# Optimization experiments

Measured on AMD Instinct MI355X. Metric: run time of the kernel, lower is better.

Reference implementation:

```python
import jax, jax.numpy as jnp
import numpy as np

TOPK = 16
MIN_SIM = 0.05
MIN_VOTES = 0.3
REMOVE_INNER = 0.5
NUM_CLASSES = 1000


def setup_inputs() -> dict:
    key = jax.random.key(0)
    kq, kdb, kid, kxy, kwh = jax.random.split(key, 5)
    Qn, N, C = 1024, 200000, 256
    q = jax.random.normal(kq, (Qn, C), dtype=jnp.float32)
    q = q / jnp.linalg.norm(q, axis=1, keepdims=True)
    db = jax.random.normal(kdb, (N, C), dtype=jnp.float32)
    db = db / jnp.linalg.norm(db, axis=1, keepdims=True)
    ids = jax.random.randint(kid, (N,), 0, NUM_CLASSES).astype(jnp.float32)
    places_db = jnp.concatenate([db, ids[:, None]], axis=1)  # (N, C+1)
    xy = jax.random.uniform(kxy, (Qn, 2), minval=0.0, maxval=800.0)
    wh = jax.random.uniform(kwh, (Qn, 2), minval=10.0, maxval=200.0)
    boxes = jnp.concatenate([xy, xy + wh], axis=1)  # valid xyxy boxes
    return {"boxes": boxes, "descriptors": q, "places_db": places_db}


def _remove_overlapping_boxes(boxes, labels, thr):
    # overlap = intersection / min(area_i, area_j); drop the BIGGER box of any
    # same-label pair whose overlap >= thr.
    bf = boxes.astype(jnp.float32)
    x1, y1, x2, y2 = bf[:, 0], bf[:, 1], bf[:, 2], bf[:, 3]
    areas = (x2 - x1) * (y2 - y1)
    xi1 = jnp.maximum(x1[:, None], x1[None, :])
    yi1 = jnp.maximum(y1[:, None], y1[None, :])
    xi2 = jnp.minimum(x2[:, None], x2[None, :])
    yi2 = jnp.minimum(y2[:, None], y2[None, :])
    inter = jnp.clip(xi2 - xi1, 0.0) * jnp.clip(yi2 - yi1, 0.0)
    area_i, area_j = areas[:, None], areas[None, :]
    area_small = jnp.minimum(area_i, area_j)
    overlap = jnp.where(area_small > 0, inter / jnp.maximum(area_small, 1e-12), 0.0)
    same_lbl = (labels[:, None] == labels[None, :]) & (labels[:, None] >= 0)
    n = boxes.shape[0]
    non_diag = ~jnp.eye(n, dtype=bool)
    mask_pair = same_lbl & (overlap >= thr) & non_diag
    bigger_i = area_i > area_j
    remove_i = (mask_pair & bigger_i).any(axis=1)
    remove_j = (mask_pair & ~bigger_i).any(axis=0)
    remove = remove_i | remove_j
    return jnp.where(remove, jnp.full_like(labels, -1), labels)


def reference(boxes, descriptors, places_db):
    X = places_db[:, :-1]                       # (N, C)
    ids = places_db[:, -1].astype(jnp.int32)    # (N,)
    sims = descriptors @ X.T                    # (Q, N)
    top_sims, top_idx = jax.lax.top_k(sims, TOPK)   # (Q, topk)
    top_ids = ids[top_idx]                          # (Q, topk)
    mask_sim = top_sims >= MIN_SIM
    # one-hot majority vote over classes
    one_hot = (top_ids[:, :, None] == jnp.arange(NUM_CLASSES, dtype=jnp.int32)[None, None, :]).astype(jnp.float32)
    vote_counts = (one_hot * mask_sim[:, :, None].astype(jnp.float32)).sum(axis=1)  # (Q, NUM_CLASSES)
    majority_counts = vote_counts.max(axis=1)
    majority_ids = jnp.argmax(vote_counts, axis=1).astype(jnp.int32)
    valid_votes = mask_sim.sum(axis=1).astype(jnp.float32)
    vote_ratio = jnp.where(valid_votes > 0, majority_counts / jnp.maximum(valid_votes, 1.0), 0.0)
    valid = (majority_counts > 0) & (vote_ratio >= MIN_VOTES)
    results = jnp.where(valid, majority_ids, jnp.full_like(majority_ids, -1))
    results = _remove_overlapping_boxes(boxes, results, REMOVE_INNER)
    match = (top_ids == results[:, None]) & mask_sim
    sim_scores = jnp.where(match, top_sims, jnp.zeros_like(top_sims)).max(axis=1)
    valid_mask = (results >= 0) & jnp.isfinite(sim_scores) & jnp.isfinite(boxes).all(axis=1)
    # Static-shape variant of the original's compaction: invalid rows are
    # marked with class=-1 / score=0 instead of being sliced out.
    return (boxes,
            jnp.where(valid_mask, sim_scores, 0.0),
            jnp.where(valid_mask, results, -1))
```

## Files before the change

kernel.cpp:

```cpp
#include <hip/hip_runtime.h>
#include <hip/hip_bf16.h>

#define QN 1024
#define NDB 200000
#define NDB_PAD 200064
#define PDBW 257
#define CDIM 256
#define TK 16
#define NEGF (-1e30f)
#define MIN_SIM_C 0.05f
#define MIN_VOTES_C 0.3f

#define NCH 128
#define THETA 0.19f
#define CAPQ 14
#define NCHUNK1 49
#define CPQ1 (NCHUNK1*32)

typedef __attribute__((ext_vector_type(8))) short bf16x8;
typedef __attribute__((ext_vector_type(4))) float f32x4;
typedef __attribute__((ext_vector_type(8))) int   i32x8;
typedef __attribute__((ext_vector_type(4))) int   i32x4;

__device__ __forceinline__ short f2bf(float f) {
  union { float f; unsigned u; } x; x.f = f;
  unsigned u = x.u;
  return (short)((u + 0x7fffu + ((u >> 16) & 1u)) >> 16);
}

__device__ __forceinline__ unsigned pk_fp8x4(float a, float b, float c, float d) {
  unsigned w = (unsigned)__builtin_amdgcn_cvt_pk_fp8_f32(a, b, 0, false);
  w = (unsigned)__builtin_amdgcn_cvt_pk_fp8_f32(c, d, (int)w, true);
  return w;
}

__global__ __launch_bounds__(512, 1) void sims_fused_kernel(
    const float* __restrict__ qd, const float* __restrict__ pdb,
    unsigned long long* __restrict__ seg_g, unsigned int* __restrict__ cnt_g,
    int* __restrict__ flag)
{
  __shared__ __align__(16) char db_lds[2][64 * 256];
  __shared__ unsigned seg_lds[8][64][CAPQ][2];
  __shared__ int lcnt[8][64];

  const int tid  = (int)threadIdx.x;
  const int lane = tid & 63;
  const int wv   = tid >> 6;
  const int cid  = (int)blockIdx.x;
  const int mt   = (int)blockIdx.y;
  const int nsub = 24 + (cid < 54 ? 1 : 0);
  const int row0 = (24*cid + (cid < 54 ? cid : 54)) << 6;

  if (cid == 0 && mt == 0 && tid == 0) *flag = 0;
  lcnt[wv][lane] = 0;

  const int l15  = lane & 15;
  const int egrp = lane >> 4;
  const int rowb = egrp << 2;
  const int colb = l15;

  const int srow = tid >> 3;
  const int sp   = tid & 7;
  const int sg0  = ((2*sp    ) ^ (srow & 15)) << 4;
  const int sg1  = ((2*sp + 1) ^ (srow & 15)) << 4;
  const int sbase = srow * 256;

  i32x8 aq[4][2];
  {
    #pragma unroll
    for (int fm = 0; fm < 4; ++fm) {
      const float* qrow = qd + (size_t)(mt*512 + wv*64 + fm*16 + l15)*CDIM;
      #pragma unroll
      for (int kk = 0; kk < 2; ++kk) {
        const float* p = qrow + kk*128 + egrp*32;
        i32x8 a;
        #pragma unroll
        for (int d = 0; d < 8; ++d) {
          float4 x = *(const float4*)(p + d*4);
          a[d] = (int)pk_fp8x4(x.x, x.y, x.z, x.w);
        }
        aq[fm][kk] = a;
      }
    }
  }

  float4 sf0, sf1, sf2, sf3, sf4, sf5, sf6, sf7;
#define LOADT(tile) do { \
    const int _r = row0 + (tile)*64 + srow; \
    if (_r < NDB) { \
      const float* _p = pdb + (size_t)_r*PDBW + sp*32; \
      sf0 = *(const float4*)(_p);      sf1 = *(const float4*)(_p + 4); \
      sf2 = *(const float4*)(_p + 8);  sf3 = *(const float4*)(_p + 12); \
      sf4 = *(const float4*)(_p + 16); sf5 = *(const float4*)(_p + 20); \
      sf6 = *(const float4*)(_p + 24); sf7 = *(const float4*)(_p + 28); \
    } else { \
      sf0 = sf1 = sf2 = sf3 = sf4 = sf5 = sf6 = sf7 = (float4){0.f, 0.f, 0.f, 0.f}; \
    } \
  } while (0)
#define STAGEW(bufi) do { \
    i32x4 _w0, _w1; \
    _w0[0] = (int)pk_fp8x4(sf0.x, sf0.y, sf0.z, sf0.w); \
    _w0[1] = (int)pk_fp8x4(sf1.x, sf1.y, sf1.z, sf1.w); \
    _w0[2] = (int)pk_fp8x4(sf2.x, sf2.y, sf2.z, sf2.w); \
    _w0[3] = (int)pk_fp8x4(sf3.x, sf3.y, sf3.z, sf3.w); \
    _w1[0] = (int)pk_fp8x4(sf4.x, sf4.y, sf4.z, sf4.w); \
    _w1[1] = (int)pk_fp8x4(sf5.x, sf5.y, sf5.z, sf5.w); \
    _w1[2] = (int)pk_fp8x4(sf6.x, sf6.y, sf6.z, sf6.w); \
    _w1[3] = (int)pk_fp8x4(sf7.x, sf7.y, sf7.z, sf7.w); \
    *(i32x4*)(db_lds[(bufi)] + sbase + sg0) = _w0; \
    *(i32x4*)(db_lds[(bufi)] + sbase + sg1) = _w1; \
  } while (0)

  LOADT(0);
  STAGEW(0);
  LOADT(1);
  __syncthreads();

  for (int s = 0; s < nsub; ++s) {
    if (s + 1 < nsub) {
      STAGEW((s + 1) & 1);
      if (s + 2 < nsub) LOADT(s + 2);
    }

    f32x4 acc[4][4];
    #pragma unroll
    for (int fm = 0; fm < 4; ++fm)
      #pragma unroll
      for (int fn = 0; fn < 4; ++fn)
        acc[fm][fn] = (f32x4){0.f, 0.f, 0.f, 0.f};
    __builtin_amdgcn_s_setprio(1);
    {
      const char* dbt = (const char*)db_lds[s & 1];
      #pragma unroll
      for (int kk = 0; kk < 2; ++kk) {
        #pragma unroll
        for (int fn = 0; fn < 4; ++fn) {
          const char* rowp = dbt + (fn*16 + l15)*256;
          const int mbase = kk*8 + egrp*2;
          i32x4 lo = *(const i32x4*)(rowp + (((mbase    ) ^ l15) << 4));
          i32x4 hi = *(const i32x4*)(rowp + (((mbase + 1) ^ l15) << 4));
          i32x8 b = __builtin_shufflevector(lo, hi, 0, 1, 2, 3, 4, 5, 6, 7);
          #pragma unroll
          for (int fm = 0; fm < 4; ++fm)
            acc[fm][fn] = __builtin_amdgcn_mfma_scale_f32_16x16x128_f8f6f4(
                aq[fm][kk], b, acc[fm][fn],
                0 , 0 ,
                0, 0x7F7F7F7Fu , 0, 0x7F7F7F7Fu );
        }
      }
    }
    __builtin_amdgcn_s_setprio(0);

    {
      const int idxbase = row0 + s*64;
      #pragma unroll
      for (int fm = 0; fm < 4; ++fm)
        #pragma unroll
        for (int fn = 0; fn < 4; ++fn) {
          const f32x4 a = acc[fm][fn];
          const float m = fmaxf(fmaxf(a[0], a[1]), fmaxf(a[2], a[3]));
          if (m > THETA) {
            #pragma unroll
            for (int j = 0; j < 4; ++j) {
              if (a[j] > THETA) {
                const int ql = fm*16 + rowb + j;
                const int slot = atomicAdd(&lcnt[wv][ql], 1);
                if (slot < CAPQ) {
                  seg_lds[wv][ql][slot][0] = __float_as_uint(a[j]);
                  seg_lds[wv][ql][slot][1] = (unsigned)(idxbase + fn*16 + colb);
                }
              }
            }
          }
        }
    }

    asm volatile("s_waitcnt lgkmcnt(0)" ::: "memory");
    __builtin_amdgcn_sched_barrier(0);
    __builtin_amdgcn_s_barrier();
    __builtin_amdgcn_sched_barrier(0);
  }
#undef LOADT
#undef STAGEW

  {
    const int cnt = lcnt[wv][lane];
    const int qg = mt*512 + wv*64 + lane;
    cnt_g[qg*NCH + cid] = (unsigned)cnt;
    const int nc = min(cnt, CAPQ);
    unsigned long long* dst = seg_g + (size_t)(qg*NCH + cid)*CAPQ;
    for (int j = 0; j < nc; ++j) {
      unsigned long long lo = seg_lds[wv][lane][j][0];
      unsigned long long hi = seg_lds[wv][lane][j][1];
      dst[j] = lo | (hi << 32);
    }
  }
}

__global__ __launch_bounds__(64) void gather_vote_kernel(
    const float* __restrict__ pdb,
    const unsigned long long* __restrict__ seg_g, const unsigned* __restrict__ cnt_g,
    int* __restrict__ out_label, float* __restrict__ out_s, int* __restrict__ flag)
{
  __shared__ float    cv[NCH*CAPQ];
  __shared__ unsigned ci[NCH*CAPQ];
  const int q    = (int)blockIdx.x;
  const int lane = (int)threadIdx.x;

  bool over = false;
  int tot = 0;
  #pragma unroll
  for (int h = 0; h < NCH/64; ++h) {
    const int c = h*64 + lane;
    const int cnt = (int)cnt_g[q*NCH + c];
    over |= (cnt > CAPQ);
    const int nc = min(cnt, CAPQ);
    tot += nc;
    const unsigned long long* src = seg_g + (size_t)(q*NCH + c)*CAPQ;
    for (int j = 0; j < CAPQ; ++j) {
      float v = NEGF; unsigned idx = 0u;
      if (j < nc) {
        const unsigned long long e = src[j];
        v = __uint_as_float((unsigned)e);
        idx = (unsigned)(e >> 32);
      }
      cv[c*CAPQ + j] = v;
      ci[c*CAPQ + j] = idx;
    }
  }
  #pragma unroll
  for (int off = 32; off >= 1; off >>= 1) tot += __shfl_xor(tot, off);
  __syncthreads();

  float topv[TK]; int topid[TK];
  #pragma unroll
  for (int r = 0; r < TK; ++r) {
    float bv = NEGF; int bp = -1;
    #pragma unroll 4
    for (int j = 0; j < (NCH*CAPQ)/64; ++j) {
      const int p = j*64 + lane;
      const float v = cv[p];
      if (v > bv) { bv = v; bp = p; }
    }
    #pragma unroll
    for (int off = 32; off >= 1; off >>= 1) {
      const float ov = __shfl_xor(bv, off);
      const int   op = __shfl_xor(bp, off);
      if (ov > bv || (ov == bv && ((unsigned)op < (unsigned)bp))) { bv = ov; bp = op; }
    }
    topv[r] = bv;
    int id = -2;
    if (bp >= 0 && bv > NEGF) id = (int)pdb[(size_t)ci[bp]*PDBW + CDIM];
    topid[r] = id;
    if (lane == 0 && bp >= 0) cv[bp] = NEGF;
    __syncthreads();
  }

  if (lane == 0) {
    bool mk[TK];
    int nvalid = 0;
    #pragma unroll
    for (int i = 0; i < TK; ++i) {
      mk[i] = (topv[i] >= MIN_SIM_C) && (topid[i] >= 0);
      nvalid += mk[i] ? 1 : 0;
    }
    int maj = 0, majid = 0x7fffffff;
    for (int i = 0; i < TK; ++i) {
      if (!mk[i]) continue;
      int c = 0;
      for (int j = 0; j < TK; ++j) c += (mk[j] && topid[j] == topid[i]) ? 1 : 0;
      if (c > maj || (c == maj && topid[i] < majid)) { maj = c; majid = topid[i]; }
    }
    const float ratio = (float)maj / fmaxf((float)nvalid, 1.0f);
    const bool valid = (maj > 0) && (ratio >= MIN_VOTES_C);
    const int label = valid ? majid : -1;
    float s = 0.f;
    #pragma unroll
    for (int i = 0; i < TK; ++i)
      if (mk[i] && topid[i] == label) s = fmaxf(s, topv[i]);
    out_label[q] = label;
    out_s[q]     = s;
  }
  const bool bad = (__ballot(over) != 0ull) || (tot < TK);
  if (lane == 0 && bad) atomicOr(flag, 1);
}

__global__ __launch_bounds__(256, 2) void sims_topk1_kernel(
    const float* __restrict__ qd, const float* __restrict__ pdb,
    float* __restrict__ cand_val, unsigned int* __restrict__ cand_idx,
    const int* __restrict__ gate)
{
  if (gate && *gate == 0) return;
  __shared__ __align__(16) short db_lds[128 * 264];
  float* sims = (float*)db_lds;

  const int tid  = (int)threadIdx.x;
  const int lane = tid & 63;
  const int wv   = tid >> 6;
  const int cid   = (int)blockIdx.x;
  const int mtile = (int)blockIdx.y;

  bf16x8 aq[2][8];
  {
    const int l15 = lane & 15;
    const int kb  = (lane >> 4) << 3;
    #pragma unroll
    for (int fm = 0; fm < 2; ++fm) {
      const int row = mtile*128 + wv*32 + fm*16 + l15;
      #pragma unroll
      for (int kk = 0; kk < 8; ++kk) {
        const float* p = qd + (size_t)row*CDIM + kk*32 + kb;
        float4 x0 = *(const float4*)p;
        float4 x1 = *(const float4*)(p + 4);
        bf16x8 a;
        a[0]=f2bf(x0.x); a[1]=f2bf(x0.y); a[2]=f2bf(x0.z); a[3]=f2bf(x0.w);
        a[4]=f2bf(x1.x); a[5]=f2bf(x1.y); a[6]=f2bf(x1.z); a[7]=f2bf(x1.w);
        aq[fm][kk] = a;
      }
    }
  }

  float    tv[TK];
  unsigned ti[TK];
  #pragma unroll
  for (int i = 0; i < TK; ++i) { tv[i] = NEGF; ti[i] = 0u; }
  float minv = NEGF; int minp = 0;

  const int g0chunk = cid * 4096;
  const int q_l  = tid & 127;
  const int half = tid >> 7;

  for (int s = 0; s < 32; ++s) {
    const int g0 = g0chunk + s*128;
    {
      const int rb = tid >> 6;
      const int c4 = (tid & 63) << 2;
      for (int i = 0; i < 32; ++i) {
        const int rl = i*4 + rb;
        const int g  = g0 + rl;
        float v0, v1, v2, v3;
        if (g < NDB) {
          const float* p = pdb + (size_t)g*PDBW + c4;
          v0 = p[0]; v1 = p[1]; v2 = p[2]; v3 = p[3];
        } else { v0 = v1 = v2 = v3 = 0.f; }
        short* d = &db_lds[rl*264 + c4];
        d[0]=f2bf(v0); d[1]=f2bf(v1); d[2]=f2bf(v2); d[3]=f2bf(v3);
      }
    }
    __syncthreads();

    f32x4 acc[2][8];
    #pragma unroll
    for (int fm = 0; fm < 2; ++fm)
      #pragma unroll
      for (int fn = 0; fn < 8; ++fn)
        acc[fm][fn] = (f32x4){0.f, 0.f, 0.f, 0.f};
    {
      const int l15 = lane & 15;
      const int kb  = (lane >> 4) << 3;
      #pragma unroll
      for (int kk = 0; kk < 8; ++kk) {
        bf16x8 b[8];
        #pragma unroll
        for (int fn = 0; fn < 8; ++fn)
          b[fn] = *(const bf16x8*)&db_lds[(fn*16 + l15)*264 + kk*32 + kb];
        #pragma unroll
        for (int fn = 0; fn < 8; ++fn) {
          acc[0][fn] = __builtin_amdgcn_mfma_f32_16x16x32_bf16(aq[0][kk], b[fn], acc[0][fn], 0, 0, 0);
          acc[1][fn] = __builtin_amdgcn_mfma_f32_16x16x32_bf16(aq[1][kk], b[fn], acc[1][fn], 0, 0, 0);
        }
      }
    }
    __syncthreads();

    {
      const int colb = lane & 15;
      const int rowb = (lane >> 4) << 2;
      #pragma unroll
      for (int fm = 0; fm < 2; ++fm)
        #pragma unroll
        for (int fn = 0; fn < 8; ++fn)
          #pragma unroll
          for (int j = 0; j < 4; ++j)
            sims[(wv*32 + fm*16 + rowb + j)*129 + fn*16 + colb] = acc[fm][fn][j];
    }
    __syncthreads();

    {
      const int cb = half * 64;
      #pragma unroll 4
      for (int c = 0; c < 64; ++c) {
        const int colc = cb + c;
        const float v = sims[q_l*129 + colc];
        const int g = g0 + colc;
        if (v > minv && g < NDB) {
          #pragma unroll
          for (int i = 0; i < TK; ++i) if (i == minp) { tv[i] = v; ti[i] = (unsigned)g; }
          minv = tv[0]; minp = 0;
          #pragma unroll
          for (int i = 1; i < TK; ++i) if (tv[i] < minv) { minv = tv[i]; minp = i; }
        }
      }
    }
    __syncthreads();
  }

  {
    const int qg = mtile*128 + q_l;
    float*    pv = cand_val + ((size_t)qg*NCHUNK1 + cid)*32 + half*TK;
    unsigned* pi = cand_idx + ((size_t)qg*NCHUNK1 + cid)*32 + half*TK;
    #pragma unroll
    for (int i = 0; i < TK; ++i) { pv[i] = tv[i]; pi[i] = ti[i]; }
  }
}

template<int CPQ>
__global__ __launch_bounds__(64) void merge_vote_kernel(
    const float* __restrict__ pdb,
    const float* __restrict__ cand_val, const unsigned* __restrict__ cand_idx,
    int* __restrict__ out_label, float* __restrict__ out_s,
    const int* __restrict__ gate)
{
  if (gate && *gate == 0) return;
  __shared__ float    cv[CPQ];
  __shared__ unsigned ci[CPQ];
  const int q    = (int)blockIdx.x;
  const int lane = (int)threadIdx.x;

  for (int j = lane; j < CPQ; j += 64) {
    cv[j] = cand_val[(size_t)q*CPQ + j];
    ci[j] = cand_idx[(size_t)q*CPQ + j];
  }
  __syncthreads();

  float topv[TK]; int topid[TK];
  #pragma unroll
  for (int r = 0; r < TK; ++r) {
    float bv = NEGF; int bp = -1;
    for (int j = lane; j < CPQ; j += 64) {
      const float v = cv[j];
      if (v > bv) { bv = v; bp = j; }
    }
    #pragma unroll
    for (int off = 32; off >= 1; off >>= 1) {
      const float ov = __shfl_xor(bv, off);
      const int   op = __shfl_xor(bp, off);
      if (ov > bv || (ov == bv && ((unsigned)op < (unsigned)bp))) { bv = ov; bp = op; }
    }
    topv[r] = bv;
    int id = -2;
    if (bp >= 0 && bv > NEGF) id = (int)pdb[(size_t)ci[bp]*PDBW + CDIM];
    topid[r] = id;
    if (lane == 0 && bp >= 0) cv[bp] = NEGF;
    __syncthreads();
  }

  if (lane == 0) {
    bool mk[TK];
    int nvalid = 0;
    #pragma unroll
    for (int i = 0; i < TK; ++i) {
      mk[i] = (topv[i] >= MIN_SIM_C) && (topid[i] >= 0);
      nvalid += mk[i] ? 1 : 0;
    }
    int maj = 0, majid = 0x7fffffff;
    for (int i = 0; i < TK; ++i) {
      if (!mk[i]) continue;
      int c = 0;
      for (int j = 0; j < TK; ++j) c += (mk[j] && topid[j] == topid[i]) ? 1 : 0;
      if (c > maj || (c == maj && topid[i] < majid)) { maj = c; majid = topid[i]; }
    }
    const float ratio = (float)maj / fmaxf((float)nvalid, 1.0f);
    const bool valid = (maj > 0) && (ratio >= MIN_VOTES_C);
    const int label = valid ? majid : -1;
    float s = 0.f;
    #pragma unroll
    for (int i = 0; i < TK; ++i)
      if (mk[i] && topid[i] == label) s = fmaxf(s, topv[i]);
    out_label[q] = label;
    out_s[q]     = s;
  }
}

__device__ __forceinline__ bool finitef(float v) {
  return ((__float_as_uint(v) >> 23) & 0xffu) != 0xffu;
}

__global__ __launch_bounds__(64) void finalize_kernel(
    const float* __restrict__ boxes, const int* __restrict__ labels,
    const float* __restrict__ svals, float* __restrict__ out)
{
  const int x    = (int)blockIdx.x;
  const int lane = (int)threadIdx.x;
  const int lx = labels[x];
  const float bx1 = boxes[x*4+0], by1 = boxes[x*4+1];
  const float bx2 = boxes[x*4+2], by2 = boxes[x*4+3];
  const float ax = (bx2 - bx1) * (by2 - by1);

  bool flag = false;
  if (lx >= 0) {
    for (int y = lane; y < QN; y += 64) {
      if (y == x) continue;
      if (labels[y] != lx) continue;
      const float c1 = boxes[y*4+0], c2 = boxes[y*4+1];
      const float c3 = boxes[y*4+2], c4 = boxes[y*4+3];
      const float ay = (c3 - c1) * (c4 - c2);
      const float xi1 = fmaxf(bx1, c1), yi1 = fmaxf(by1, c2);
      const float xi2 = fminf(bx2, c3), yi2 = fminf(by2, c4);
      const float inter = fmaxf(xi2 - xi1, 0.f) * fmaxf(yi2 - yi1, 0.f);
      const float asmall = fminf(ax, ay);
      const float ov = (asmall > 0.f) ? inter / fmaxf(asmall, 1e-12f) : 0.f;
      if (ov >= 0.5f && ay <= ax) flag = true;
    }
  }
  const bool removed = (__ballot(flag) != 0ull);
  const int label = removed ? -1 : lx;
  const float s = svals[x];
  const bool fin = finitef(s) && finitef(bx1) && finitef(by1) && finitef(bx2) && finitef(by2);
  const bool valid = (label >= 0) && fin;

  if (lane == 0) {
    out[4096 + x] = valid ? s : 0.f;
    out[5120 + x] = (float)(valid ? label : -1);
  }
  if (lane < 4) out[x*4 + lane] = boxes[x*4 + lane];
}

extern "C" void kernel_launch(void* const* d_in, const int* in_sizes, int n_in,
                              void* d_out, int out_size, void* d_ws, size_t ws_size,
                              hipStream_t stream)
{
  const float* boxes = (const float*)d_in[0];
  const float* qd    = (const float*)d_in[1];
  const float* pdb   = (const float*)d_in[2];
  float* out = (float*)d_out;
  char* ws = (char*)d_ws;

  const size_t seg_bytes = (size_t)QN * NCH * CAPQ * 8;
  const size_t cnt_bytes = (size_t)QN * NCH * 4;
  const size_t c1_bytes  = (size_t)QN * CPQ1 * 8;
  const size_t A_bytes   = (seg_bytes + cnt_bytes > c1_bytes) ? seg_bytes + cnt_bytes : c1_bytes;
  const size_t need = A_bytes + (size_t)QN*8 + 64;

  if (ws_size >= need) {
    char* A = ws;
    unsigned long long* seg_g = (unsigned long long*)A;
    unsigned*           cnt_g = (unsigned*)(A + seg_bytes);
    float*    cand_val = (float*)A;
    unsigned* cand_idx = (unsigned*)(A + (size_t)QN*CPQ1*4);
    int*      labels   = (int*)(ws + A_bytes);
    float*    svals    = (float*)(ws + A_bytes + (size_t)QN*4);
    int*      flag     = (int*)(ws + A_bytes + (size_t)QN*8);

    hipLaunchKernelGGL(sims_fused_kernel, dim3(NCH, 2), dim3(512), 0, stream,
                       qd, pdb, seg_g, cnt_g, flag);
    hipLaunchKernelGGL(gather_vote_kernel, dim3(QN), dim3(64), 0, stream,
                       pdb, seg_g, cnt_g, labels, svals, flag);
    hipLaunchKernelGGL(sims_topk1_kernel, dim3(NCHUNK1, 8), dim3(256), 0, stream,
                       qd, pdb, cand_val, cand_idx, flag);
    hipLaunchKernelGGL((merge_vote_kernel<CPQ1>), dim3(QN), dim3(64), 0, stream,
                       pdb, cand_val, cand_idx, labels, svals, flag);
    hipLaunchKernelGGL(finalize_kernel, dim3(QN), dim3(64), 0, stream,
                       boxes, labels, svals, out);
  } else {
    const size_t n1 = (size_t)QN * CPQ1;
    float*    cand_val = (float*)ws;
    unsigned* cand_idx = (unsigned*)(ws + n1*4);
    int*      labels   = (int*)(ws + n1*8);
    float*    svals    = (float*)(ws + n1*8 + (size_t)QN*4);

    hipLaunchKernelGGL(sims_topk1_kernel, dim3(NCHUNK1, 8), dim3(256), 0, stream,
                       qd, pdb, cand_val, cand_idx, (const int*)nullptr);
    hipLaunchKernelGGL((merge_vote_kernel<CPQ1>), dim3(QN), dim3(64), 0, stream,
                       pdb, cand_val, cand_idx, labels, svals, (const int*)nullptr);
    hipLaunchKernelGGL(finalize_kernel, dim3(QN), dim3(64), 0, stream,
                       boxes, labels, svals, out);
  }
}
```

Measured before the change: 157.0 us.

## Process 128-row superstep per barrier with double-prefetched halves and split staging

The main loop now handles two 64-row tiles per iteration with a four-buffer LDS ring. Staging of the next tile and issuing of the global prefetch are interleaved between the two MFMA halves, which halves the number of block barriers. Launch bounds change from one block per CU to waves_per_eu(2,2). This doubles the staging LDS footprint and doubles the prefetch registers held in flight. Register pressure rises and the occupancy hint may be incompatible with the LDS use.

```diff
diff --git a/kernel.cpp b/kernel.cpp
--- a/kernel.cpp
+++ b/kernel.cpp
@@ -34,12 +34,40 @@
   return w;
 }
 
-__global__ __launch_bounds__(512, 1) void sims_fused_kernel(
+__device__ __forceinline__ void loadh(float4 (&P)[8], const float* __restrict__ pdb,
+                                      int r, int sp) {
+  if (r < NDB) {
+    const float* p = pdb + (size_t)r*PDBW + sp*32;
+    #pragma unroll
+    for (int i = 0; i < 8; ++i) P[i] = *(const float4*)(p + i*4);
+  } else {
+    #pragma unroll
+    for (int i = 0; i < 8; ++i) P[i] = (float4){0.f, 0.f, 0.f, 0.f};
+  }
+}
+
+__device__ __forceinline__ void stageh(const float4 (&P)[8], char* __restrict__ buf,
+                                       int sbase, int sg0, int sg1) {
+  i32x4 w0, w1;
+  w0[0] = (int)pk_fp8x4(P[0].x, P[0].y, P[0].z, P[0].w);
+  w0[1] = (int)pk_fp8x4(P[1].x, P[1].y, P[1].z, P[1].w);
+  w0[2] = (int)pk_fp8x4(P[2].x, P[2].y, P[2].z, P[2].w);
+  w0[3] = (int)pk_fp8x4(P[3].x, P[3].y, P[3].z, P[3].w);
+  w1[0] = (int)pk_fp8x4(P[4].x, P[4].y, P[4].z, P[4].w);
+  w1[1] = (int)pk_fp8x4(P[5].x, P[5].y, P[5].z, P[5].w);
+  w1[2] = (int)pk_fp8x4(P[6].x, P[6].y, P[6].z, P[6].w);
+  w1[3] = (int)pk_fp8x4(P[7].x, P[7].y, P[7].z, P[7].w);
+  *(i32x4*)(buf + sbase + sg0) = w0;
+  *(i32x4*)(buf + sbase + sg1) = w1;
+}
+
+__global__ __launch_bounds__(512) __attribute__((amdgpu_waves_per_eu(2, 2)))
+void sims_fused_kernel(
     const float* __restrict__ qd, const float* __restrict__ pdb,
     unsigned long long* __restrict__ seg_g, unsigned int* __restrict__ cnt_g,
     int* __restrict__ flag)
 {
-  __shared__ __align__(16) char db_lds[2][64 * 256];
+  __shared__ __align__(16) char db_lds[4][64 * 256];
   __shared__ unsigned seg_lds[8][64][CAPQ][2];
   __shared__ int lcnt[8][64];
 
@@ -48,8 +76,8 @@
   const int wv   = tid >> 6;
   const int cid  = (int)blockIdx.x;
   const int mt   = (int)blockIdx.y;
-  const int nsub = 24 + (cid < 54 ? 1 : 0);
-  const int row0 = (24*cid + (cid < 54 ? cid : 54)) << 6;
+  const int nsub = 12 + (cid < 27 ? 1 : 0);
+  const int row0 = (12*cid + (cid < 27 ? cid : 27)) << 7;
 
   if (cid == 0 && mt == 0 && tid == 0) *flag = 0;
   lcnt[wv][lane] = 0;
@@ -84,104 +112,98 @@
     }
   }
 
-  float4 sf0, sf1, sf2, sf3, sf4, sf5, sf6, sf7;
-#define LOADT(tile) do { \
-    const int _r = row0 + (tile)*64 + srow; \
-    if (_r < NDB) { \
-      const float* _p = pdb + (size_t)_r*PDBW + sp*32; \
-      sf0 = *(const float4*)(_p);      sf1 = *(const float4*)(_p + 4); \
-      sf2 = *(const float4*)(_p + 8);  sf3 = *(const float4*)(_p + 12); \
-      sf4 = *(const float4*)(_p + 16); sf5 = *(const float4*)(_p + 20); \
-      sf6 = *(const float4*)(_p + 24); sf7 = *(const float4*)(_p + 28); \
-    } else { \
-      sf0 = sf1 = sf2 = sf3 = sf4 = sf5 = sf6 = sf7 = (float4){0.f, 0.f, 0.f, 0.f}; \
+  float4 sfA[8], sfB[8];
+
+#define MFMA_HALF(bufi) do { \
+    const char* dbt = (const char*)db_lds[(bufi)]; \
+    _Pragma("unroll") \
+    for (int kk = 0; kk < 2; ++kk) { \
+      _Pragma("unroll") \
+      for (int fn = 0; fn < 4; ++fn) { \
+        const char* rowp = dbt + (fn*16 + l15)*256; \
+        const int mbase = kk*8 + egrp*2; \
+        i32x4 lo = *(const i32x4*)(rowp + (((mbase    ) ^ l15) << 4)); \
+        i32x4 hi = *(const i32x4*)(rowp + (((mbase + 1) ^ l15) << 4)); \
+        i32x8 b = __builtin_shufflevector(lo, hi, 0, 1, 2, 3, 4, 5, 6, 7); \
+        _Pragma("unroll") \
+        for (int fm = 0; fm < 4; ++fm) \
+          acc[fm][fn] = __builtin_amdgcn_mfma_scale_f32_16x16x128_f8f6f4( \
+              aq[fm][kk], b, acc[fm][fn], 0, 0, 0, 0x7F7F7F7Fu, 0, 0x7F7F7F7Fu); \
+      } \
     } \
   } while (0)
-#define STAGEW(bufi) do { \
-    i32x4 _w0, _w1; \
-    _w0[0] = (int)pk_fp8x4(sf0.x, sf0.y, sf0.z, sf0.w); \
-    _w0[1] = (int)pk_fp8x4(sf1.x, sf1.y, sf1.z, sf1.w); \
-    _w0[2] = (int)pk_fp8x4(sf2.x, sf2.y, sf2.z, sf2.w); \
-    _w0[3] = (int)pk_fp8x4(sf3.x, sf3.y, sf3.z, sf3.w); \
-    _w1[0] = (int)pk_fp8x4(sf4.x, sf4.y, sf4.z, sf4.w); \
-    _w1[1] = (int)pk_fp8x4(sf5.x, sf5.y, sf5.z, sf5.w); \
-    _w1[2] = (int)pk_fp8x4(sf6.x, sf6.y, sf6.z, sf6.w); \
-    _w1[3] = (int)pk_fp8x4(sf7.x, sf7.y, sf7.z, sf7.w); \
-    *(i32x4*)(db_lds[(bufi)] + sbase + sg0) = _w0; \
-    *(i32x4*)(db_lds[(bufi)] + sbase + sg1) = _w1; \
+#define FILTER_HALF(idxbase) do { \
+    _Pragma("unroll") \
+    for (int fm = 0; fm < 4; ++fm) \
+      _Pragma("unroll") \
+      for (int fn = 0; fn < 4; ++fn) { \
+        const f32x4 a = acc[fm][fn]; \
+        const float m = fmaxf(fmaxf(a[0], a[1]), fmaxf(a[2], a[3])); \
+        if (m > THETA) { \
+          _Pragma("unroll") \
+          for (int j = 0; j < 4; ++j) { \
+            if (a[j] > THETA) { \
+              const int ql = fm*16 + rowb + j; \
+              const int slot = atomicAdd(&lcnt[wv][ql], 1); \
+              if (slot < CAPQ) { \
+                seg_lds[wv][ql][slot][0] = __float_as_uint(a[j]); \
+                seg_lds[wv][ql][slot][1] = (unsigned)((idxbase) + fn*16 + colb); \
+              } \
+            } \
+          } \
+        } \
+      } \
   } while (0)
 
-  LOADT(0);
-  STAGEW(0);
-  LOADT(1);
+  loadh(sfA, pdb, row0 + srow, sp);
+  loadh(sfB, pdb, row0 + 64 + srow, sp);
+  stageh(sfA, db_lds[0], sbase, sg0, sg1);
+  stageh(sfB, db_lds[1], sbase, sg0, sg1);
+  loadh(sfA, pdb, row0 + 128 + srow, sp);
+  loadh(sfB, pdb, row0 + 192 + srow, sp);
   __syncthreads();
 
   for (int s = 0; s < nsub; ++s) {
+    const int R0 = (s & 1) << 1;
+    const int W0 = ((s & 1) ^ 1) << 1;
+
+    f32x4 acc[4][4];
+    #pragma unroll
+    for (int fm = 0; fm < 4; ++fm)
+      #pragma unroll
+      for (int fn = 0; fn < 4; ++fn)
+        acc[fm][fn] = (f32x4){0.f, 0.f, 0.f, 0.f};
+
+    __builtin_amdgcn_s_setprio(1);
+    MFMA_HALF(R0);
+    __builtin_amdgcn_s_setprio(0);
     if (s + 1 < nsub) {
-      STAGEW((s + 1) & 1);
-      if (s + 2 < nsub) LOADT(s + 2);
-    }
-
-    f32x4 acc[4][4];
+      stageh(sfA, db_lds[W0], sbase, sg0, sg1);
+      if (s + 2 < nsub) loadh(sfA, pdb, row0 + (s+2)*128 + srow, sp);
+    }
+    FILTER_HALF(row0 + s*128);
+
     #pragma unroll
     for (int fm = 0; fm < 4; ++fm)
       #pragma unroll
       for (int fn = 0; fn < 4; ++fn)
         acc[fm][fn] = (f32x4){0.f, 0.f, 0.f, 0.f};
     __builtin_amdgcn_s_setprio(1);
-    {
-      const char* dbt = (const char*)db_lds[s & 1];
-      #pragma unroll
-      for (int kk = 0; kk < 2; ++kk) {
-        #pragma unroll
-        for (int fn = 0; fn < 4; ++fn) {
-          const char* rowp = dbt + (fn*16 + l15)*256;
-          const int mbase = kk*8 + egrp*2;
-          i32x4 lo = *(const i32x4*)(rowp + (((mbase    ) ^ l15) << 4));
-          i32x4 hi = *(const i32x4*)(rowp + (((mbase + 1) ^ l15) << 4));
-          i32x8 b = __builtin_shufflevector(lo, hi, 0, 1, 2, 3, 4, 5, 6, 7);
-          #pragma unroll
-          for (int fm = 0; fm < 4; ++fm)
-            acc[fm][fn] = __builtin_amdgcn_mfma_scale_f32_16x16x128_f8f6f4(
-                aq[fm][kk], b, acc[fm][fn],
-                0 , 0 ,
-                0, 0x7F7F7F7Fu , 0, 0x7F7F7F7Fu );
-        }
-      }
-    }
+    MFMA_HALF(R0 + 1);
     __builtin_amdgcn_s_setprio(0);
-
-    {
-      const int idxbase = row0 + s*64;
-      #pragma unroll
-      for (int fm = 0; fm < 4; ++fm)
-        #pragma unroll
-        for (int fn = 0; fn < 4; ++fn) {
-          const f32x4 a = acc[fm][fn];
-          const float m = fmaxf(fmaxf(a[0], a[1]), fmaxf(a[2], a[3]));
-          if (m > THETA) {
-            #pragma unroll
-            for (int j = 0; j < 4; ++j) {
-              if (a[j] > THETA) {
-                const int ql = fm*16 + rowb + j;
-                const int slot = atomicAdd(&lcnt[wv][ql], 1);
-                if (slot < CAPQ) {
-                  seg_lds[wv][ql][slot][0] = __float_as_uint(a[j]);
-                  seg_lds[wv][ql][slot][1] = (unsigned)(idxbase + fn*16 + colb);
-                }
-              }
-            }
-          }
-        }
-    }
+    if (s + 1 < nsub) {
+      stageh(sfB, db_lds[W0 + 1], sbase, sg0, sg1);
+      if (s + 2 < nsub) loadh(sfB, pdb, row0 + (s+2)*128 + 64 + srow, sp);
+    }
+    FILTER_HALF(row0 + s*128 + 64);
 
     asm volatile("s_waitcnt lgkmcnt(0)" ::: "memory");
     __builtin_amdgcn_sched_barrier(0);
     __builtin_amdgcn_s_barrier();
     __builtin_amdgcn_sched_barrier(0);
   }
-#undef LOADT
-#undef STAGEW
+#undef MFMA_HALF
+#undef FILTER_HALF
 
   {
     const int cnt = lcnt[wv][lane];
```

Result: slower. 181.4 us (+15.5%).

## Halve per-block query tile and double grid y-dimension in fused sims kernel

Applied to the files above, without the earlier changes.

Each block of the fused similarity kernel now handles 256 queries (32 per wave) instead of 512, and the grid grows from 128x2 to 128x4 blocks. This puts more blocks on the GPU, cuts per-wave accumulator and register use, and halves the shared candidate buffers. The trade-off is that each database tile is now loaded from global memory and converted to fp8 twice as often across blocks. The load and stage macros are also replaced by inline helper functions.

```diff
diff --git a/kernel.cpp b/kernel.cpp
--- a/kernel.cpp
+++ b/kernel.cpp
@@ -34,14 +34,41 @@
   return w;
 }
 
+__device__ __forceinline__ void loadh(float4 (&P)[8], const float* __restrict__ pdb,
+                                      int r, int sp) {
+  if (r < NDB) {
+    const float* p = pdb + (size_t)r*PDBW + sp*32;
+    #pragma unroll
+    for (int i = 0; i < 8; ++i) P[i] = *(const float4*)(p + i*4);
+  } else {
+    #pragma unroll
+    for (int i = 0; i < 8; ++i) P[i] = (float4){0.f, 0.f, 0.f, 0.f};
+  }
+}
+
+__device__ __forceinline__ void stageh(const float4 (&P)[8], char* __restrict__ buf,
+                                       int sbase, int sg0, int sg1) {
+  i32x4 w0, w1;
+  w0[0] = (int)pk_fp8x4(P[0].x, P[0].y, P[0].z, P[0].w);
+  w0[1] = (int)pk_fp8x4(P[1].x, P[1].y, P[1].z, P[1].w);
+  w0[2] = (int)pk_fp8x4(P[2].x, P[2].y, P[2].z, P[2].w);
+  w0[3] = (int)pk_fp8x4(P[3].x, P[3].y, P[3].z, P[3].w);
+  w1[0] = (int)pk_fp8x4(P[4].x, P[4].y, P[4].z, P[4].w);
+  w1[1] = (int)pk_fp8x4(P[5].x, P[5].y, P[5].z, P[5].w);
+  w1[2] = (int)pk_fp8x4(P[6].x, P[6].y, P[6].z, P[6].w);
+  w1[3] = (int)pk_fp8x4(P[7].x, P[7].y, P[7].z, P[7].w);
+  *(i32x4*)(buf + sbase + sg0) = w0;
+  *(i32x4*)(buf + sbase + sg1) = w1;
+}
+
 __global__ __launch_bounds__(512, 1) void sims_fused_kernel(
     const float* __restrict__ qd, const float* __restrict__ pdb,
     unsigned long long* __restrict__ seg_g, unsigned int* __restrict__ cnt_g,
     int* __restrict__ flag)
 {
   __shared__ __align__(16) char db_lds[2][64 * 256];
-  __shared__ unsigned seg_lds[8][64][CAPQ][2];
-  __shared__ int lcnt[8][64];
+  __shared__ unsigned seg_lds[8][32][CAPQ][2];
+  __shared__ int lcnt[8][32];
 
   const int tid  = (int)threadIdx.x;
   const int lane = tid & 63;
@@ -52,7 +79,7 @@
   const int row0 = (24*cid + (cid < 54 ? cid : 54)) << 6;
 
   if (cid == 0 && mt == 0 && tid == 0) *flag = 0;
-  lcnt[wv][lane] = 0;
+  if (lane < 32) lcnt[wv][lane] = 0;
 
   const int l15  = lane & 15;
   const int egrp = lane >> 4;
@@ -65,11 +92,11 @@
   const int sg1  = ((2*sp + 1) ^ (srow & 15)) << 4;
   const int sbase = srow * 256;
 
-  i32x8 aq[4][2];
+  i32x8 aq[2][2];
   {
     #pragma unroll
-    for (int fm = 0; fm < 4; ++fm) {
-      const float* qrow = qd + (size_t)(mt*512 + wv*64 + fm*16 + l15)*CDIM;
+    for (int fm = 0; fm < 2; ++fm) {
+      const float* qrow = qd + (size_t)(mt*256 + wv*32 + fm*16 + l15)*CDIM;
       #pragma unroll
       for (int kk = 0; kk < 2; ++kk) {
         const float* p = qrow + kk*128 + egrp*32;
@@ -84,47 +111,22 @@
     }
   }
 
-  float4 sf0, sf1, sf2, sf3, sf4, sf5, sf6, sf7;
-#define LOADT(tile) do { \
-    const int _r = row0 + (tile)*64 + srow; \
-    if (_r < NDB) { \
-      const float* _p = pdb + (size_t)_r*PDBW + sp*32; \
-      sf0 = *(const float4*)(_p);      sf1 = *(const float4*)(_p + 4); \
-      sf2 = *(const float4*)(_p + 8);  sf3 = *(const float4*)(_p + 12); \
-      sf4 = *(const float4*)(_p + 16); sf5 = *(const float4*)(_p + 20); \
-      sf6 = *(const float4*)(_p + 24); sf7 = *(const float4*)(_p + 28); \
-    } else { \
-      sf0 = sf1 = sf2 = sf3 = sf4 = sf5 = sf6 = sf7 = (float4){0.f, 0.f, 0.f, 0.f}; \
-    } \
-  } while (0)
-#define STAGEW(bufi) do { \
-    i32x4 _w0, _w1; \
-    _w0[0] = (int)pk_fp8x4(sf0.x, sf0.y, sf0.z, sf0.w); \
-    _w0[1] = (int)pk_fp8x4(sf1.x, sf1.y, sf1.z, sf1.w); \
-    _w0[2] = (int)pk_fp8x4(sf2.x, sf2.y, sf2.z, sf2.w); \
-    _w0[3] = (int)pk_fp8x4(sf3.x, sf3.y, sf3.z, sf3.w); \
-    _w1[0] = (int)pk_fp8x4(sf4.x, sf4.y, sf4.z, sf4.w); \
-    _w1[1] = (int)pk_fp8x4(sf5.x, sf5.y, sf5.z, sf5.w); \
-    _w1[2] = (int)pk_fp8x4(sf6.x, sf6.y, sf6.z, sf6.w); \
-    _w1[3] = (int)pk_fp8x4(sf7.x, sf7.y, sf7.z, sf7.w); \
-    *(i32x4*)(db_lds[(bufi)] + sbase + sg0) = _w0; \
-    *(i32x4*)(db_lds[(bufi)] + sbase + sg1) = _w1; \
-  } while (0)
-
-  LOADT(0);
-  STAGEW(0);
-  LOADT(1);
+  float4 sf[8];
+
+  loadh(sf, pdb, row0 + srow, sp);
+  stageh(sf, db_lds[0], sbase, sg0, sg1);
+  loadh(sf, pdb, row0 + 64 + srow, sp);
   __syncthreads();
 
   for (int s = 0; s < nsub; ++s) {
     if (s + 1 < nsub) {
-      STAGEW((s + 1) & 1);
-      if (s + 2 < nsub) LOADT(s + 2);
-    }
-
-    f32x4 acc[4][4];
-    #pragma unroll
-    for (int fm = 0; fm < 4; ++fm)
+      stageh(sf, db_lds[(s + 1) & 1], sbase, sg0, sg1);
+      if (s + 2 < nsub) loadh(sf, pdb, row0 + (s+2)*64 + srow, sp);
+    }
+
+    f32x4 acc[2][4];
+    #pragma unroll
+    for (int fm = 0; fm < 2; ++fm)
       #pragma unroll
       for (int fn = 0; fn < 4; ++fn)
         acc[fm][fn] = (f32x4){0.f, 0.f, 0.f, 0.f};
@@ -141,7 +143,7 @@
           i32x4 hi = *(const i32x4*)(rowp + (((mbase + 1) ^ l15) << 4));
           i32x8 b = __builtin_shufflevector(lo, hi, 0, 1, 2, 3, 4, 5, 6, 7);
           #pragma unroll
-          for (int fm = 0; fm < 4; ++fm)
+          for (int fm = 0; fm < 2; ++fm)
             acc[fm][fn] = __builtin_amdgcn_mfma_scale_f32_16x16x128_f8f6f4(
                 aq[fm][kk], b, acc[fm][fn],
                 0 , 0 ,
@@ -154,7 +156,7 @@
     {
       const int idxbase = row0 + s*64;
       #pragma unroll
-      for (int fm = 0; fm < 4; ++fm)
+      for (int fm = 0; fm < 2; ++fm)
         #pragma unroll
         for (int fn = 0; fn < 4; ++fn) {
           const f32x4 a = acc[fm][fn];
@@ -180,12 +182,10 @@
     __builtin_amdgcn_s_barrier();
     __builtin_amdgcn_sched_barrier(0);
   }
-#undef LOADT
-#undef STAGEW
-
-  {
+
+  if (lane < 32) {
     const int cnt = lcnt[wv][lane];
-    const int qg = mt*512 + wv*64 + lane;
+    const int qg = mt*256 + wv*32 + lane;
     cnt_g[qg*NCH + cid] = (unsigned)cnt;
     const int nc = min(cnt, CAPQ);
     unsigned long long* dst = seg_g + (size_t)(qg*NCH + cid)*CAPQ;
@@ -552,7 +552,7 @@
     float*    svals    = (float*)(ws + A_bytes + (size_t)QN*4);
     int*      flag     = (int*)(ws + A_bytes + (size_t)QN*8);
 
-    hipLaunchKernelGGL(sims_fused_kernel, dim3(NCH, 2), dim3(512), 0, stream,
+    hipLaunchKernelGGL(sims_fused_kernel, dim3(NCH, 4), dim3(512), 0, stream,
                        qd, pdb, seg_g, cnt_g, flag);
     hipLaunchKernelGGL(gather_vote_kernel, dim3(QN), dim3(64), 0, stream,
                        pdb, seg_g, cnt_g, labels, svals, flag);
```

After: 176.6 us. +12.5%, slower.
